# Performance work log

Hardware: AMD Instinct MI355X
Metric: run time of the kernel (lower is better)

The kernel has to match this reference:

```python
import jax, jax.numpy as jnp
import numpy as np

# MoE config (matches init_kwargs)
E = 32      # num_experts
K = 4       # num_experts_per_tok (top_k)
H = 1024    # hidden_size
I = 512     # moe_intermediate_size (shared expert uses I * num_shared_experts = I)
B, S = 2, 2048
T = B * S
C = 1024
ROUTED_SCALE = 1.0


def _silu_and_mul(gu):
    g, u = jnp.split(gu, 2, axis=-1)
    return jax.nn.silu(g) * u


def setup_inputs() -> dict:
    key = jax.random.key(0)
    ks = jax.random.split(key, 6)
    s = 0.02
    return {
        "hidden_states": jax.random.normal(ks[0], (B, S, H), jnp.float32),
        "gate_w": jax.random.normal(ks[1], (E, H), jnp.float32) * s,
        "w_gate_up": jax.random.normal(ks[2], (E, H, 2 * I), jnp.float32) * s,
        "w_down": jax.random.normal(ks[3], (E, I, H), jnp.float32) * s,
        "shared_w_gate_up": jax.random.normal(ks[4], (H, 2 * I), jnp.float32) * s,
        "shared_w_down": jax.random.normal(ks[5], (I, H), jnp.float32) * s,
    }


def reference(hidden_states, gate_w, w_gate_up, w_down, shared_w_gate_up, shared_w_down):
    b, s, h = hidden_states.shape
    x = hidden_states.reshape(-1, h)                      # [T, H]
    t = x.shape[0]

    # --- router: gate linear -> softmax -> top-k -> renormalize ---
    logits = x @ gate_w.T                                 # [T, E]
    probs = jax.nn.softmax(logits, axis=-1)
    topk_w, topk_idx = jax.lax.top_k(probs, K)            # [T, K]
    topk_w = topk_w / jnp.sum(topk_w, axis=-1, keepdims=True)  # norm_topk_prob
    topk_w = topk_w * ROUTED_SCALE

    # --- dispatch: sort (token, slot) assignments by expert, scatter into capacity buffer ---
    e_flat = topk_idx.reshape(-1)                         # [T*K]
    w_flat = topk_w.reshape(-1)
    t_flat = jnp.repeat(jnp.arange(t), K)
    order = jnp.argsort(e_flat)                           # stable sort by expert id
    e_s, w_s, t_s = e_flat[order], w_flat[order], t_flat[order]
    counts = jax.ops.segment_sum(jnp.ones_like(e_s), e_s, num_segments=E)
    starts = jnp.cumsum(counts) - counts                  # exclusive prefix sum
    pos = jnp.arange(t * K) - starts[e_s]                 # position within expert group
    slot = jnp.minimum(pos, C)                            # overflow -> trash slot C
    buf = jnp.zeros((E, C + 1, h), x.dtype).at[e_s, slot].set(x[t_s])

    # --- grouped expert MLP (silu-gated) ---
    gu = jnp.einsum('ech,ehi->eci', buf[:, :C], w_gate_up)        # [E, C, 2I]
    expert_out = jnp.einsum('eci,eih->ech', _silu_and_mul(gu), w_down)  # [E, C, H]
    expert_out = jnp.pad(expert_out, ((0, 0), (0, 1), (0, 0)))    # trash slot reads zero

    # --- combine: gather back, weight, scatter-add per token ---
    gate = jnp.where(pos < C, w_s, 0.0)[:, None]
    routed = jnp.zeros_like(x).at[t_s].add(expert_out[e_s, slot] * gate)

    # --- shared expert MLP ---
    shared = _silu_and_mul(x @ shared_w_gate_up) @ shared_w_down

    return (routed + shared).reshape(b, s, h)
```

## Files before the change

kernel.cpp:

```cpp
#include <hip/hip_runtime.h>
#include <cstdint>
#include <cstddef>

#define NEXP   32
#define TOPK   4
#define HD     1024
#define ID     512
#define TT     4096
#define CAP    1024
#define SHARED_BASE (NEXP*CAP)
#define NSLOT  (NEXP*CAP + TT)

#define KSPLIT 16
#define KCH    64
#define KSUB   32

typedef __attribute__((ext_vector_type(4))) float f32x4;
typedef __bf16 bf16x8 __attribute__((ext_vector_type(8)));

__device__ __forceinline__ unsigned short f2bf(float f) {
    union { float f; unsigned int u; } v; v.f = f;
    unsigned int u = v.u;
    u = (u + 0x7FFFu + ((u >> 16) & 1u)) >> 16;
    return (unsigned short)u;
}
__device__ __forceinline__ float bf2f(unsigned short s) {
    union { unsigned int u; float f; } v; v.u = ((unsigned int)s) << 16;
    return v.f;
}

#define GLOAD_LDS16(g, l)                                                     \
    __builtin_amdgcn_global_load_lds(                                         \
        (__attribute__((address_space(1))) void*)(g),                         \
        (__attribute__((address_space(3))) void*)(l), 16, 0, 0)

__global__ void k_convert_x(const float* __restrict__ src,
                            unsigned short* __restrict__ dst, int n4) {
    int i = blockIdx.x * blockDim.x + threadIdx.x;
    if (i >= n4) return;
    float4 v = ((const float4*)src)[i];
    ushort4 o;
    o.x = f2bf(v.x); o.y = f2bf(v.y); o.z = f2bf(v.z); o.w = f2bf(v.w);
    ((ushort4*)dst)[i] = o;
}

__global__ void k_transpose_bf16(const float* __restrict__ src,
                                 unsigned short* __restrict__ dst,
                                 int K, int N) {
    __shared__ float ld[64][65];
    const size_t esz = (size_t)K * N;
    src += (size_t)blockIdx.z * esz;
    dst += (size_t)blockIdx.z * esz;
    const int n0 = blockIdx.x * 64, k0 = blockIdx.y * 64;
    const int tid = threadIdx.x;
    const int c4 = (tid & 15) * 4;
    const int rbase = tid >> 4;
#pragma unroll
    for (int p = 0; p < 4; p++) {
        int row = rbase + p * 16;
        float4 v = *(const float4*)(src + (size_t)(k0 + row) * N + n0 + c4);
        ld[row][c4 + 0] = v.x; ld[row][c4 + 1] = v.y;
        ld[row][c4 + 2] = v.z; ld[row][c4 + 3] = v.w;
    }
    __syncthreads();
    const int n  = tid >> 2;
    const int ks = (tid & 3) * 16;
    unsigned short tmp[16];
#pragma unroll
    for (int i = 0; i < 16; i++) tmp[i] = f2bf(ld[ks + i][n]);
    uint4 a, b;
    a.x = tmp[0] | (tmp[1] << 16);  a.y = tmp[2] | (tmp[3] << 16);
    a.z = tmp[4] | (tmp[5] << 16);  a.w = tmp[6] | (tmp[7] << 16);
    b.x = tmp[8] | (tmp[9] << 16);  b.y = tmp[10] | (tmp[11] << 16);
    b.z = tmp[12] | (tmp[13] << 16); b.w = tmp[14] | (tmp[15] << 16);
    unsigned short* op = dst + (size_t)(n0 + n) * K + k0 + ks;
    *(uint4*)op = a;
    *(uint4*)(op + 8) = b;
}

__global__ __launch_bounds__(256)
void k_logits(const float* __restrict__ x, const float* __restrict__ gw,
              float* __restrict__ part) {
    __shared__ float xsT[KSUB][260];
    __shared__ float gsT[KSUB][36];
    const int tid = threadIdx.x;
    const int lane = tid & 63, wv = tid >> 6;
    const int tg = lane >> 2, eg = lane & 3;
    const int t0 = blockIdx.x * 256;
    const int kbase = blockIdx.y * KCH;
    const int tbase = wv * 64 + tg * 4;
    const int ebase = eg * 8;

    float acc[4][8];
#pragma unroll
    for (int j = 0; j < 4; j++)
#pragma unroll
        for (int i = 0; i < 8; i++) acc[j][i] = 0.f;

    for (int ks = 0; ks < KCH; ks += KSUB) {
        const int k0 = kbase + ks;
        if (ks > 0) __syncthreads();
#pragma unroll
        for (int p = 0; p < 8; p++) {
            int vid = p * 256 + tid;
            int t = vid >> 3, kq = (vid & 7) * 4;
            float4 v = *(const float4*)(x + (size_t)(t0 + t) * HD + k0 + kq);
            xsT[kq + 0][t] = v.x; xsT[kq + 1][t] = v.y;
            xsT[kq + 2][t] = v.z; xsT[kq + 3][t] = v.w;
        }
#pragma unroll
        for (int p = 0; p < 4; p++) {
            int vid = p * 256 + tid;
            int e = vid >> 5, k = vid & 31;
            gsT[k][e] = gw[(size_t)e * HD + k0 + k];
        }
        __syncthreads();
#pragma unroll 4
        for (int k = 0; k < KSUB; k++) {
            float4 xv = *(const float4*)&xsT[k][tbase];
            float4 g0 = *(const float4*)&gsT[k][ebase];
            float4 g1 = *(const float4*)&gsT[k][ebase + 4];
            float xa[4] = {xv.x, xv.y, xv.z, xv.w};
#pragma unroll
            for (int j = 0; j < 4; j++) {
                acc[j][0] += xa[j] * g0.x; acc[j][1] += xa[j] * g0.y;
                acc[j][2] += xa[j] * g0.z; acc[j][3] += xa[j] * g0.w;
                acc[j][4] += xa[j] * g1.x; acc[j][5] += xa[j] * g1.y;
                acc[j][6] += xa[j] * g1.z; acc[j][7] += xa[j] * g1.w;
            }
        }
    }
    const size_t base = ((size_t)blockIdx.y * TT + (t0 + tbase)) * 32 + ebase;
#pragma unroll
    for (int j = 0; j < 4; j++) {
        float4 w0, w1;
        w0.x = acc[j][0]; w0.y = acc[j][1]; w0.z = acc[j][2]; w0.w = acc[j][3];
        w1.x = acc[j][4]; w1.y = acc[j][5]; w1.z = acc[j][6]; w1.w = acc[j][7];
        *(float4*)(part + base + (size_t)j * 32) = w0;
        *(float4*)(part + base + (size_t)j * 32 + 4) = w1;
    }
}

__global__ __launch_bounds__(256)
void k_topk(const float* __restrict__ part,
            int* __restrict__ choice, float* __restrict__ cw,
            int* __restrict__ tok, float* __restrict__ wgt) {
    const int lane = threadIdx.x & 63, wv = threadIdx.x >> 6;
    const int t = blockIdx.x * 4 + wv;
    const int e = lane & 31;
    const int sbase = (lane >> 5) * 8;
    float v = 0.f;
#pragma unroll
    for (int s = 0; s < 8; s++)
        v += part[((size_t)(sbase + s) * TT + t) * 32 + e];
    v += __shfl_xor(v, 32);
    float sc = (lane < 32) ? v : -INFINITY;

    float lv[TOPK]; int le[TOPK];
#pragma unroll
    for (int r = 0; r < TOPK; r++) {
        float m = sc;
#pragma unroll
        for (int d = 1; d < 64; d <<= 1) m = fmaxf(m, __shfl_xor(m, d));
        unsigned long long ball = __ballot(sc == m);
        int widx = __ffsll(ball) - 1;
        lv[r] = m; le[r] = widx;
        if (lane == widx) sc = -INFINITY;
    }
    if (lane == 0) {
        float wv4[TOPK], wsum = 0.f;
#pragma unroll
        for (int r = 0; r < TOPK; r++) { wv4[r] = __expf(lv[r] - lv[0]); wsum += wv4[r]; }
#pragma unroll
        for (int r = 0; r < TOPK; r++) {
            choice[t * TOPK + r] = le[r];
            cw[t * TOPK + r] = wv4[r] / wsum;
        }
        tok[SHARED_BASE + t] = t;
        wgt[SHARED_BASE + t] = 1.0f;
    }
}

__global__ __launch_bounds__(1024)
void k_assign(const int* __restrict__ choice, const float* __restrict__ cw,
              int* __restrict__ cnt, int* __restrict__ tok,
              float* __restrict__ wgt, int* __restrict__ smap) {
    const int e = blockIdx.x;
    const int tid = threadIdx.x, lane = tid & 63, wv = tid >> 6;
    __shared__ int wtot[16];
    int running = 0;
    for (int it = 0; it < (TT * TOPK) / 1024; it++) {
        const int i = it * 1024 + tid;
        const bool match = (choice[i] == e);
        unsigned long long ball = __ballot(match);
        int wt = __popcll(ball);
        int wpre = __popcll(ball & ((1ull << lane) - 1ull));
        if (lane == 0) wtot[wv] = wt;
        __syncthreads();
        int woff = 0, tot = 0;
#pragma unroll
        for (int w = 0; w < 16; w++) { int c = wtot[w]; tot += c; if (w < wv) woff += c; }
        int pos = running + woff + wpre;
        running += tot;
        __syncthreads();
        if (match) {
            if (pos < CAP) {
                int slot = e * CAP + pos;
                tok[slot] = i >> 2;
                wgt[slot] = cw[i];
                smap[i] = slot;
            } else {
                smap[i] = -1;
            }
        }
    }
    if (tid == 0) cnt[e] = min(running, CAP);
}

template <int KD, bool GATHER, bool SILU>
__global__ __launch_bounds__(256)
void k_moe_gemm(const unsigned short* __restrict__ Ab,
                const unsigned short* __restrict__ Bt,
                unsigned short* __restrict__ Cout,
                const int* __restrict__ tok,
                const int* __restrict__ cnt) {
    const int mwork = blockIdx.y;
    int e, mt;
    if (mwork < 256) { e = mwork >> 3; mt = mwork & 7; }
    else             { e = NEXP;       mt = mwork - 256; }
    const int slotbase = (e < NEXP) ? e * CAP : SHARED_BASE;
    const int cE = (e < NEXP) ? min(cnt[e], CAP) : TT;
    const int m0 = mt * 128;
    if (m0 >= cE) return;
    const int rowsv = min(128, cE - m0);
    const int nt = blockIdx.x;

    const unsigned short* Bte = Bt + (size_t)e * (1024 * KD);

    __shared__ unsigned short As[128 * 32];
    __shared__ unsigned short Bs[128 * 32];

    const int tid  = threadIdx.x;
    const int lane = tid & 63;
    const int wv   = tid >> 6;

    const int rr  = lane >> 2;
    const int seg = (lane & 3) ^ ((lane >> 3) & 3);
    const int r0 = wv * 32 + rr;
    const int r1 = r0 + 16;

    int ga0 = m0 + r0, ga1 = m0 + r1;
    int ra0, ra1;
    if (GATHER) {
        ra0 = (ga0 < cE) ? tok[slotbase + ga0] : 0;
        ra1 = (ga1 < cE) ? tok[slotbase + ga1] : 0;
    } else {
        ra0 = slotbase + ga0;
        ra1 = slotbase + ga1;
    }
    const unsigned short* ap0 = Ab + (size_t)ra0 * KD + seg * 8;
    const unsigned short* ap1 = Ab + (size_t)ra1 * KD + seg * 8;

    int br0, br1;
    if (SILU) {
        int in0 = r0 & 63, in1 = r1 & 63;
        int c0 = nt * 64 + (r0 >> 6) * 32 + (in0 & 31);
        int c1 = nt * 64 + (r1 >> 6) * 32 + (in1 & 31);
        br0 = (in0 < 32) ? c0 : 512 + c0;
        br1 = (in1 < 32) ? c1 : 512 + c1;
    } else {
        br0 = nt * 128 + r0;
        br1 = nt * 128 + r1;
    }
    const unsigned short* bp0 = Bte + (size_t)br0 * KD + seg * 8;
    const unsigned short* bp1 = Bte + (size_t)br1 * KD + seg * 8;

    unsigned short* asd0 = As + (wv * 32) * 32;
    unsigned short* asd1 = As + (wv * 32 + 16) * 32;
    unsigned short* bsd0 = Bs + (wv * 32) * 32;
    unsigned short* bsd1 = Bs + (wv * 32 + 16) * 32;

    f32x4 acc[4][4];
#pragma unroll
    for (int i = 0; i < 4; i++)
#pragma unroll
        for (int j = 0; j < 4; j++) acc[i][j] = (f32x4)(0.0f);

    const int mrow = lane & 15;
    const int quad = lane >> 4;
    const int wm = wv >> 1, wn = wv & 1;
    const int sw = (quad ^ ((mrow >> 1) & 3)) * 8;

    const unsigned short* aRd = As + (wm * 64 + mrow) * 32 + sw;
    const unsigned short* bRd = Bs + (wn * 64 + mrow) * 32 + sw;

    for (int k0 = 0; k0 < KD; k0 += 32) {
        GLOAD_LDS16(ap0 + k0, asd0);
        GLOAD_LDS16(ap1 + k0, asd1);
        GLOAD_LDS16(bp0 + k0, bsd0);
        GLOAD_LDS16(bp1 + k0, bsd1);
        __syncthreads();
        bf16x8 af[4], bf[4];
#pragma unroll
        for (int i = 0; i < 4; i++) {
            af[i] = *(const bf16x8*)(aRd + i * 16 * 32);
            bf[i] = *(const bf16x8*)(bRd + i * 16 * 32);
        }
#pragma unroll
        for (int mi = 0; mi < 4; mi++)
#pragma unroll
            for (int nj = 0; nj < 4; nj++)
                acc[mi][nj] = __builtin_amdgcn_mfma_f32_16x16x32_bf16(
                    af[mi], bf[nj], acc[mi][nj], 0, 0, 0);
        __syncthreads();
    }

    if (SILU) {
#pragma unroll
        for (int mi = 0; mi < 4; mi++)
#pragma unroll
            for (int nj = 0; nj < 2; nj++) {
                f32x4 g = acc[mi][nj];
                f32x4 u = acc[mi][nj + 2];
#pragma unroll
                for (int r = 0; r < 4; r++) {
                    int rloc = wm * 64 + mi * 16 + quad * 4 + r;
                    if (rloc < rowsv) {
                        float gv = g[r], uv = u[r];
                        float a = (gv / (1.f + __expf(-gv))) * uv;
                        int c = nt * 64 + wn * 32 + nj * 16 + mrow;
                        Cout[(size_t)(slotbase + m0 + rloc) * ID + c] = f2bf(a);
                    }
                }
            }
    } else {
#pragma unroll
        for (int mi = 0; mi < 4; mi++)
#pragma unroll
            for (int nj = 0; nj < 4; nj++) {
                f32x4 v = acc[mi][nj];
#pragma unroll
                for (int r = 0; r < 4; r++) {
                    int rloc = wm * 64 + mi * 16 + quad * 4 + r;
                    if (rloc < rowsv) {
                        int c = nt * 128 + wn * 64 + nj * 16 + mrow;
                        Cout[(size_t)(slotbase + m0 + rloc) * HD + c] = f2bf(v[r]);
                    }
                }
            }
    }
}

__global__ __launch_bounds__(256)
void k_combine(const unsigned short* __restrict__ eout,
               const int* __restrict__ smap,
               const float* __restrict__ wgt,
               float* __restrict__ out) {
    const int t = blockIdx.x;
    const int h0 = threadIdx.x * 4;
    ushort4 q = *(const ushort4*)(eout + (size_t)(SHARED_BASE + t) * HD + h0);
    float a0 = bf2f(q.x), a1 = bf2f(q.y), a2 = bf2f(q.z), a3 = bf2f(q.w);
#pragma unroll
    for (int r = 0; r < TOPK; r++) {
        int slot = smap[t * TOPK + r];
        if (slot >= 0) {
            float w = wgt[slot];
            ushort4 e4 = *(const ushort4*)(eout + (size_t)slot * HD + h0);
            a0 += w * bf2f(e4.x); a1 += w * bf2f(e4.y);
            a2 += w * bf2f(e4.z); a3 += w * bf2f(e4.w);
        }
    }
    float4 o; o.x = a0; o.y = a1; o.z = a2; o.w = a3;
    *(float4*)(out + (size_t)t * HD + h0) = o;
}

extern "C" void kernel_launch(void* const* d_in, const int* in_sizes, int n_in,
                              void* d_out, int out_size, void* d_ws, size_t ws_size,
                              hipStream_t stream) {
    const float* x   = (const float*)d_in[0];
    const float* gw  = (const float*)d_in[1];
    const float* wgu = (const float*)d_in[2];
    const float* wdn = (const float*)d_in[3];
    const float* sgu = (const float*)d_in[4];
    const float* sdn = (const float*)d_in[5];
    float* out = (float*)d_out;

    char* w = (char*)d_ws;
    size_t off = 0;
    int* cnt = (int*)(w + off);                       off += 256;
    unsigned short* xb     = (unsigned short*)(w + off); off += (size_t)TT * HD * 2;
    unsigned short* wgup_t = (unsigned short*)(w + off); off += (size_t)33 * 1024 * 1024 * 2;
    unsigned short* wdn_t  = (unsigned short*)(w + off); off += (size_t)33 * 1024 * 512 * 2;
    unsigned short* act    = (unsigned short*)(w + off); off += (size_t)NSLOT * ID * 2;
    unsigned short* eout   = (unsigned short*)(w + off); off += (size_t)NSLOT * HD * 2;
    int*   tok    = (int*)(w + off);   off += (size_t)NSLOT * 4;
    float* wgt    = (float*)(w + off); off += (size_t)NSLOT * 4;
    int*   smap   = (int*)(w + off);   off += (size_t)TT * TOPK * 4;
    int*   choice = (int*)(w + off);   off += (size_t)TT * TOPK * 4;
    float* cw     = (float*)(w + off); off += (size_t)TT * TOPK * 4;

    float* part = (float*)eout;

    k_convert_x<<<(TT * HD / 4 + 255) / 256, 256, 0, stream>>>(x, xb, TT * HD / 4);

    k_transpose_bf16<<<dim3(16, 16, 32), 256, 0, stream>>>(wgu, wgup_t, 1024, 1024);
    k_transpose_bf16<<<dim3(16, 16, 1),  256, 0, stream>>>(sgu, wgup_t + (size_t)32 * 1024 * 1024, 1024, 1024);
    k_transpose_bf16<<<dim3(16, 8, 32),  256, 0, stream>>>(wdn, wdn_t, 512, 1024);
    k_transpose_bf16<<<dim3(16, 8, 1),   256, 0, stream>>>(sdn, wdn_t + (size_t)32 * 1024 * 512, 512, 1024);

    k_logits<<<dim3(16, KSPLIT), 256, 0, stream>>>(x, gw, part);
    k_topk<<<TT / 4, 256, 0, stream>>>(part, choice, cw, tok, wgt);
    k_assign<<<NEXP, 1024, 0, stream>>>(choice, cw, cnt, tok, wgt, smap);

    k_moe_gemm<1024, true, true><<<dim3(8, 288), 256, 0, stream>>>(xb, wgup_t, act, tok, cnt);
    k_moe_gemm<512, false, false><<<dim3(8, 288), 256, 0, stream>>>(act, wdn_t, eout, tok, cnt);

    k_combine<<<TT, 256, 0, stream>>>(eout, smap, wgt, out);
}
```

Measured before the change: 453.2 us.

## Double-buffer LDS in MoE GEMM and launch over compacted expert tile list

Adds a small kernel that builds a compact list of (expert, m-tile) work items from expert counts, so GEMM blocks index only non-empty tiles instead of early-exiting. The GEMM main loop now double-buffers the A/B shared tiles, issuing the next k-slice's global-to-LDS loads before computing the current one and dropping one barrier per iteration. This aims to overlap memory latency with MFMA work, at the cost of doubled LDS usage and an extra tiny serial launch.

```diff
diff --git a/kernel.cpp b/kernel.cpp
--- a/kernel.cpp
+++ b/kernel.cpp
@@ -10,6 +10,7 @@
 #define CAP    1024
 #define SHARED_BASE (NEXP*CAP)
 #define NSLOT  (NEXP*CAP + TT)
+#define MAXTILES 320
 
 #define KSPLIT 16
 #define KCH    64
@@ -217,28 +218,41 @@
     if (tid == 0) cnt[e] = min(running, CAP);
 }
 
+__global__ void k_tiles(const int* __restrict__ cnt,
+                        int* __restrict__ tiles, int* __restrict__ ntiles) {
+    if (threadIdx.x != 0) return;
+    int j = 0;
+    for (int e = 0; e <= NEXP; e++) {
+        int c = (e < NEXP) ? min(cnt[e], CAP) : TT;
+        int nt = (c + 127) >> 7;
+        for (int mt = 0; mt < nt; mt++) tiles[j++] = (e << 8) | mt;
+    }
+    *ntiles = j;
+}
+
 template <int KD, bool GATHER, bool SILU>
 __global__ __launch_bounds__(256)
 void k_moe_gemm(const unsigned short* __restrict__ Ab,
                 const unsigned short* __restrict__ Bt,
                 unsigned short* __restrict__ Cout,
                 const int* __restrict__ tok,
-                const int* __restrict__ cnt) {
-    const int mwork = blockIdx.y;
-    int e, mt;
-    if (mwork < 256) { e = mwork >> 3; mt = mwork & 7; }
-    else             { e = NEXP;       mt = mwork - 256; }
+                const int* __restrict__ cnt,
+                const int* __restrict__ tiles,
+                const int* __restrict__ ntiles) {
+    const int j = blockIdx.y;
+    if (j >= *ntiles) return;
+    const int packed = tiles[j];
+    const int e = packed >> 8, mt = packed & 255;
     const int slotbase = (e < NEXP) ? e * CAP : SHARED_BASE;
     const int cE = (e < NEXP) ? min(cnt[e], CAP) : TT;
     const int m0 = mt * 128;
-    if (m0 >= cE) return;
     const int rowsv = min(128, cE - m0);
     const int nt = blockIdx.x;
 
     const unsigned short* Bte = Bt + (size_t)e * (1024 * KD);
 
-    __shared__ unsigned short As[128 * 32];
-    __shared__ unsigned short Bs[128 * 32];
+    __shared__ unsigned short As[2][128 * 32];
+    __shared__ unsigned short Bs[2][128 * 32];
 
     const int tid  = threadIdx.x;
     const int lane = tid & 63;
@@ -275,36 +289,42 @@
     const unsigned short* bp0 = Bte + (size_t)br0 * KD + seg * 8;
     const unsigned short* bp1 = Bte + (size_t)br1 * KD + seg * 8;
 
-    unsigned short* asd0 = As + (wv * 32) * 32;
-    unsigned short* asd1 = As + (wv * 32 + 16) * 32;
-    unsigned short* bsd0 = Bs + (wv * 32) * 32;
-    unsigned short* bsd1 = Bs + (wv * 32 + 16) * 32;
+    const int aoff0 = (wv * 32) * 32, aoff1 = (wv * 32 + 16) * 32;
 
     f32x4 acc[4][4];
 #pragma unroll
     for (int i = 0; i < 4; i++)
 #pragma unroll
-        for (int j = 0; j < 4; j++) acc[i][j] = (f32x4)(0.0f);
+        for (int j2 = 0; j2 < 4; j2++) acc[i][j2] = (f32x4)(0.0f);
 
     const int mrow = lane & 15;
     const int quad = lane >> 4;
     const int wm = wv >> 1, wn = wv & 1;
     const int sw = (quad ^ ((mrow >> 1) & 3)) * 8;
 
-    const unsigned short* aRd = As + (wm * 64 + mrow) * 32 + sw;
-    const unsigned short* bRd = Bs + (wn * 64 + mrow) * 32 + sw;
-
+    const int aRdOff = (wm * 64 + mrow) * 32 + sw;
+    const int bRdOff = (wn * 64 + mrow) * 32 + sw;
+
+    GLOAD_LDS16(ap0, As[0] + aoff0);
+    GLOAD_LDS16(ap1, As[0] + aoff1);
+    GLOAD_LDS16(bp0, Bs[0] + aoff0);
+    GLOAD_LDS16(bp1, Bs[0] + aoff1);
+
+    int p = 0;
     for (int k0 = 0; k0 < KD; k0 += 32) {
-        GLOAD_LDS16(ap0 + k0, asd0);
-        GLOAD_LDS16(ap1 + k0, asd1);
-        GLOAD_LDS16(bp0 + k0, bsd0);
-        GLOAD_LDS16(bp1 + k0, bsd1);
         __syncthreads();
+        if (k0 + 32 < KD) {
+            const int kn = k0 + 32;
+            GLOAD_LDS16(ap0 + kn, As[p ^ 1] + aoff0);
+            GLOAD_LDS16(ap1 + kn, As[p ^ 1] + aoff1);
+            GLOAD_LDS16(bp0 + kn, Bs[p ^ 1] + aoff0);
+            GLOAD_LDS16(bp1 + kn, Bs[p ^ 1] + aoff1);
+        }
         bf16x8 af[4], bf[4];
 #pragma unroll
         for (int i = 0; i < 4; i++) {
-            af[i] = *(const bf16x8*)(aRd + i * 16 * 32);
-            bf[i] = *(const bf16x8*)(bRd + i * 16 * 32);
+            af[i] = *(const bf16x8*)(As[p] + aRdOff + i * 16 * 32);
+            bf[i] = *(const bf16x8*)(Bs[p] + bRdOff + i * 16 * 32);
         }
 #pragma unroll
         for (int mi = 0; mi < 4; mi++)
@@ -312,7 +332,7 @@
             for (int nj = 0; nj < 4; nj++)
                 acc[mi][nj] = __builtin_amdgcn_mfma_f32_16x16x32_bf16(
                     af[mi], bf[nj], acc[mi][nj], 0, 0, 0);
-        __syncthreads();
+        p ^= 1;
     }
 
     if (SILU) {
@@ -398,6 +418,8 @@
     int*   smap   = (int*)(w + off);   off += (size_t)TT * TOPK * 4;
     int*   choice = (int*)(w + off);   off += (size_t)TT * TOPK * 4;
     float* cw     = (float*)(w + off); off += (size_t)TT * TOPK * 4;
+    int*   tiles  = (int*)(w + off);   off += (size_t)MAXTILES * 4;
+    int*   ntiles = (int*)(w + off);   off += 256;
 
     float* part = (float*)eout;
 
@@ -411,9 +433,10 @@
     k_logits<<<dim3(16, KSPLIT), 256, 0, stream>>>(x, gw, part);
     k_topk<<<TT / 4, 256, 0, stream>>>(part, choice, cw, tok, wgt);
     k_assign<<<NEXP, 1024, 0, stream>>>(choice, cw, cnt, tok, wgt, smap);
-
-    k_moe_gemm<1024, true, true><<<dim3(8, 288), 256, 0, stream>>>(xb, wgup_t, act, tok, cnt);
-    k_moe_gemm<512, false, false><<<dim3(8, 288), 256, 0, stream>>>(act, wdn_t, eout, tok, cnt);
+    k_tiles<<<1, 64, 0, stream>>>(cnt, tiles, ntiles);
+
+    k_moe_gemm<1024, true, true><<<dim3(8, MAXTILES), 256, 0, stream>>>(xb, wgup_t, act, tok, cnt, tiles, ntiles);
+    k_moe_gemm<512, false, false><<<dim3(8, MAXTILES), 256, 0, stream>>>(act, wdn_t, eout, tok, cnt, tiles, ntiles);
 
     k_combine<<<TT, 256, 0, stream>>>(eout, smap, wgt, out);
 }
```

Result: no change. 450.5 us (-0.6%).
